# Performance work log

Measured on AMD Instinct MI355X. Metric: run time of the kernel, lower is better.

## Reference

```python
import jax, jax.numpy as jnp
import numpy as np

NEG_SLOPE = 0.2   # PyG GATConv default negative_slope
NUM_GRAPHS = 64   # graphs per batched timestep (max batch id + 1)


def setup_inputs() -> dict:
    key = jax.random.key(0)
    ks = jax.random.split(key, 16)
    T, N, E, F, H, C, B = 8, 20000, 320000, 128, 128, 16, NUM_GRAPHS
    x = jax.random.normal(ks[0], (T, N, F), dtype=jnp.float32)
    edge_index = jax.random.randint(ks[1], (T, 2, E), 0, N, dtype=jnp.int32)
    batch = jnp.sort(jax.random.randint(ks[2], (N,), 0, B, dtype=jnp.int32))
    z = jax.random.normal(ks[3], (B, H), dtype=jnp.float32)
    s_f = 1.0 / np.sqrt(F)
    s_h = 1.0 / np.sqrt(H)
    return {
        "x": x, "edge_index": edge_index, "batch": batch, "z": z,
        "gat_W": jax.random.normal(ks[4], (F, H), jnp.float32) * s_f,
        "att_src": jax.random.normal(ks[5], (H,), jnp.float32) * s_h,
        "att_dst": jax.random.normal(ks[6], (H,), jnp.float32) * s_h,
        "gat_bias": jnp.zeros((H,), jnp.float32),
        "W_ih": jax.random.normal(ks[7], (4 * H, H), jnp.float32) * s_h,
        "W_hh": jax.random.normal(ks[8], (4 * H, H), jnp.float32) * s_h,
        "b_ih": jnp.zeros((4 * H,), jnp.float32),
        "b_hh": jnp.zeros((4 * H,), jnp.float32),
        "fc_W": jax.random.normal(ks[9], (C, 2 * H), jnp.float32) * (1.0 / np.sqrt(2 * H)),
        "fc_b": jnp.zeros((C,), jnp.float32),
    }


def _gat_conv(x, edge_index, W, a_src, a_dst, bias):
    # PyG GATConv, heads=1, add_self_loops=True: gather -> softmax-per-target -> scatter
    N = x.shape[0]
    h = x @ W                                        # [N, H]
    loops = jnp.arange(N, dtype=edge_index.dtype)
    src = jnp.concatenate([edge_index[0], loops])    # message source j
    dst = jnp.concatenate([edge_index[1], loops])    # message target i
    e = jax.nn.leaky_relu((h @ a_src)[src] + (h @ a_dst)[dst], NEG_SLOPE)  # [E+N]
    m = jax.ops.segment_max(e, dst, num_segments=N)  # stable softmax over incoming edges
    w = jnp.exp(e - m[dst])
    denom = jax.ops.segment_sum(w, dst, num_segments=N)
    alpha = w / denom[dst]
    out = jax.ops.segment_sum(alpha[:, None] * h[src], dst, num_segments=N)
    return out + bias


def reference(x, edge_index, batch, z, gat_W, att_src, att_dst, gat_bias,
              W_ih, W_hh, b_ih, b_hh, fc_W, fc_b):
    B = NUM_GRAPHS
    # per-timestep GAT (vmapped over the window) + global mean pool
    node_feats = jax.vmap(lambda xt, ei: _gat_conv(xt, ei, gat_W, att_src, att_dst, gat_bias))(x, edge_index)  # [T,N,H]
    counts = jnp.maximum(jax.ops.segment_sum(jnp.ones_like(batch, jnp.float32), batch, num_segments=B), 1.0)
    pooled = jax.vmap(lambda f: jax.ops.segment_sum(f, batch, num_segments=B))(node_feats) / counts[None, :, None]  # [T,B,H]

    # LSTM over T (PyTorch gate order i, f, g, o)
    H = gat_W.shape[1]
    h0 = jnp.zeros((B, H), x.dtype)

    def step(carry, xt):
        h, c = carry
        gates = xt @ W_ih.T + b_ih + h @ W_hh.T + b_hh
        i, f, g, o = jnp.split(gates, 4, axis=-1)
        c = jax.nn.sigmoid(f) * c + jax.nn.sigmoid(i) * jnp.tanh(g)
        h = jax.nn.sigmoid(o) * jnp.tanh(c)
        return (h, c), None

    (h_n, _), _ = jax.lax.scan(step, (h0, h0), pooled)
    # dropout is identity at inference
    return jnp.concatenate([h_n, z], axis=1) @ fc_W.T + fc_b  # [B, num_classes]
```

## Files before the change

kernel.cpp:

```cpp
#include <hip/hip_runtime.h>
#include <math.h>

#define TT 8
#define NNODES 20000
#define NEDGES 320000
#define FDIM 128
#define HDIM 128
#define BGR 64
#define NCLS 16
#define NB 157
#define CB 80
#define EC 4000
#define CAP 2816

__device__ __forceinline__ float lrelu(float x) { return fmaxf(x, 0.2f * x); }
__device__ __forceinline__ float sigmoidf(float x) { return 1.0f / (1.0f + __expf(-x)); }
__device__ __forceinline__ float tanh_fast(float x) {
  return 1.0f - 2.0f / (__expf(2.0f * x) + 1.0f);
}
__device__ __forceinline__ unsigned short f2bf(float f) {
  unsigned int u = __float_as_uint(f);
  unsigned int r = (u + 0x7fff + ((u >> 16) & 1)) >> 16;
  return (unsigned short)r;
}
__device__ __forceinline__ float bf_lo(unsigned int u) { return __uint_as_float(u << 16); }
__device__ __forceinline__ float bf_hi(unsigned int u) { return __uint_as_float(u & 0xffff0000u); }

__global__ __launch_bounds__(256) void k_prep(
    const float* __restrict__ W, const float* __restrict__ att_s, const float* __restrict__ att_d,
    float* __restrict__ u, float* __restrict__ v) {
  const int tid = threadIdx.x;
  if (tid < 128) {
    float su = 0.f, sv = 0.f;
    const float4* wr = (const float4*)(W + (size_t)tid * 128);
    #pragma unroll 8
    for (int q = 0; q < 32; ++q) {
      float4 w4 = wr[q];
      float4 a4 = *(const float4*)(att_s + q * 4);
      float4 d4 = *(const float4*)(att_d + q * 4);
      su += w4.x * a4.x + w4.y * a4.y + w4.z * a4.z + w4.w * a4.w;
      sv += w4.x * d4.x + w4.y * d4.y + w4.z * d4.z + w4.w * d4.w;
    }
    u[tid] = su; v[tid] = sv;
  }
}

__global__ __launch_bounds__(256) void k_gemv(
    const float* __restrict__ x, const float* __restrict__ u, const float* __restrict__ v,
    float* __restrict__ as_, float* __restrict__ ad_, float* __restrict__ denom,
    unsigned int* __restrict__ xb) {
  const int tid = threadIdx.x;
  const int c4 = tid & 31;
  const int ty = tid >> 5;
  const int lane = tid & 63;
  float4 uu = *(const float4*)(u + c4 * 4);
  float4 vv = *(const float4*)(v + c4 * 4);
  const int base = blockIdx.x * 64;
  #pragma unroll
  for (int it = 0; it < 8; ++it) {
    int r = base + it * 8 + ty;
    float4 xv = *(const float4*)(x + (size_t)r * FDIM + c4 * 4);
    float ps = xv.x * uu.x + xv.y * uu.y + xv.z * uu.z + xv.w * uu.w;
    float pd = xv.x * vv.x + xv.y * vv.y + xv.z * vv.z + xv.w * vv.w;
    float4 px;
    px.x = __shfl_xor(xv.x, 16);
    px.y = __shfl_xor(xv.y, 16);
    px.z = __shfl_xor(xv.z, 16);
    px.w = __shfl_xor(xv.w, 16);
    if (c4 < 16) {
      uint4 pk;
      pk.x = (unsigned int)f2bf(xv.x) | ((unsigned int)f2bf(px.x) << 16);
      pk.y = (unsigned int)f2bf(xv.y) | ((unsigned int)f2bf(px.y) << 16);
      pk.z = (unsigned int)f2bf(xv.z) | ((unsigned int)f2bf(px.z) << 16);
      pk.w = (unsigned int)f2bf(xv.w) | ((unsigned int)f2bf(px.w) << 16);
      *(uint4*)(xb + (size_t)r * 64 + c4 * 4) = pk;
    }
    #pragma unroll
    for (int o = 16; o > 0; o >>= 1) { ps += __shfl_xor(ps, o); pd += __shfl_xor(pd, o); }
    if ((lane & 31) == 0) {
      as_[r] = ps;
      ad_[r] = pd;
      denom[r] = __expf(lrelu(ps + pd));
    }
  }
}

__global__ __launch_bounds__(256) void k_scat(
    const int* __restrict__ ei, int* __restrict__ cnt_d, int* __restrict__ cnt_s,
    unsigned int* __restrict__ part_d, unsigned int* __restrict__ part_s) {
  __shared__ unsigned int buf[EC];
  __shared__ int hd[NB], hs[NB];
  __shared__ int bd[NB], bs[NB];
  const int tid = threadIdx.x;
  const int chunk = blockIdx.x, t = blockIdx.y;
  if (tid < NB) { hd[tid] = 0; hs[tid] = 0; }
  __syncthreads();
  const int* eis = ei + (size_t)t * 2 * NEDGES;
  for (int i = tid; i < EC; i += 256) {
    int e = chunk * EC + i;
    int s = eis[e], d = eis[NEDGES + e];
    buf[i] = ((unsigned int)s << 15) | (unsigned int)d;
    atomicAdd(&hd[d >> 7], 1);
    atomicAdd(&hs[s >> 7], 1);
  }
  __syncthreads();
  if (tid < NB) {
    bd[tid] = atomicAdd(&cnt_d[t * NB + tid], hd[tid]);
    bs[tid] = atomicAdd(&cnt_s[t * NB + tid], hs[tid]);
    hd[tid] = 0; hs[tid] = 0;
  }
  __syncthreads();
  unsigned int* pdt = part_d + (size_t)t * NB * CAP;
  unsigned int* pst = part_s + (size_t)t * NB * CAP;
  for (int i = tid; i < EC; i += 256) {
    unsigned int rec = buf[i];
    int d = rec & 32767, s = rec >> 15;
    int Bd = d >> 7, Bs = s >> 7;
    int od = bd[Bd] + atomicAdd(&hd[Bd], 1);
    pdt[Bd * CAP + od] = rec;
    int os = bs[Bs] + atomicAdd(&hs[Bs], 1);
    pst[Bs * CAP + os] = rec;
  }
}

__global__ __launch_bounds__(256) void k_denomB(
    const unsigned int* __restrict__ part_d, const int* __restrict__ cnt_d,
    const float* __restrict__ as_, const float* __restrict__ ad_,
    const float* __restrict__ dseed, const int* __restrict__ batch,
    float4* __restrict__ aux4, int* __restrict__ starts) {
  __shared__ float hist[128];
  __shared__ float adl[128];
  const int tid = threadIdx.x;
  const int B = blockIdx.x, t = blockIdx.y;
  if (tid < 128) {
    hist[tid] = 0.f;
    int n = B * 128 + tid;
    adl[tid] = (n < NNODES) ? ad_[t * NNODES + n] : 0.f;
  }
  __syncthreads();
  const int cnt = cnt_d[t * NB + B];
  const unsigned int* pdt = part_d + ((size_t)t * NB + B) * CAP;
  const float* asb = as_ + (size_t)t * NNODES;
  int i = tid;
  for (; i + 768 < cnt; i += 1024) {
    unsigned int r0 = pdt[i], r1 = pdt[i + 256], r2 = pdt[i + 512], r3 = pdt[i + 768];
    float v0 = asb[r0 >> 15], v1 = asb[r1 >> 15], v2 = asb[r2 >> 15], v3 = asb[r3 >> 15];
    float w0 = __expf(lrelu(v0 + adl[r0 & 127]));
    float w1 = __expf(lrelu(v1 + adl[r1 & 127]));
    float w2 = __expf(lrelu(v2 + adl[r2 & 127]));
    float w3 = __expf(lrelu(v3 + adl[r3 & 127]));
    atomicAdd(&hist[r0 & 127], w0);
    atomicAdd(&hist[r1 & 127], w1);
    atomicAdd(&hist[r2 & 127], w2);
    atomicAdd(&hist[r3 & 127], w3);
  }
  for (; i < cnt; i += 256) {
    unsigned int rec = pdt[i];
    float w = __expf(lrelu(asb[rec >> 15] + adl[rec & 127]));
    atomicAdd(&hist[rec & 127], w);
  }
  __syncthreads();
  if (tid < 128) {
    int n = B * 128 + tid;
    if (n < NNODES) {
      float den = dseed[t * NNODES + n] + hist[tid];
      int bn = batch[n];
      aux4[t * NNODES + n] = make_float4(adl[tid], 1.0f / den, __int_as_float(bn), 0.f);
      if (t == 0) {
        if (n == 0) { for (int bb = 0; bb <= bn; ++bb) starts[bb] = 0; }
        else { int pb = batch[n - 1]; for (int bb = pb + 1; bb <= bn; ++bb) starts[bb] = n; }
        if (n == NNODES - 1) { for (int bb = bn + 1; bb <= BGR; ++bb) starts[bb] = NNODES; }
      }
    }
  }
}

__global__ __launch_bounds__(256) void k_cpgemm(
    const unsigned int* __restrict__ part_s, const int* __restrict__ cnt_s,
    const float* __restrict__ as_, const float4* __restrict__ aux4,
    const unsigned int* __restrict__ xb, unsigned int* __restrict__ ppart) {
  __shared__ float clT[128 * 64];
  const int tid = threadIdx.x;
  const int lane = tid & 63;
  const int B = blockIdx.x, t = blockIdx.y;
  #pragma unroll
  for (int i = tid; i < 128 * 64; i += 256) clT[i] = 0.f;
  const float* asb = as_ + (size_t)t * NNODES;
  float a0 = asb[min(B * 128 + lane, NNODES - 1)];
  float a1 = asb[min(B * 128 + 64 + lane, NNODES - 1)];
  __syncthreads();
  const float4* auxt = aux4 + (size_t)t * NNODES;
  if (tid < 128) {
    int n = B * 128 + tid;
    if (n < NNODES) {
      float4 aa = auxt[n];
      float wself = __expf(lrelu(asb[n] + aa.x)) * aa.y;
      atomicAdd(&clT[tid * 64 + __float_as_int(aa.z)], wself);
    }
  }
  {
    const int cnt = cnt_s[t * NB + B];
    const unsigned int* pst = part_s + ((size_t)t * NB + B) * CAP;
    int i = tid;
    for (; i + 768 < cnt; i += 1024) {
      unsigned int r0 = pst[i], r1 = pst[i + 256], r2 = pst[i + 512], r3 = pst[i + 768];
      float4 x0 = auxt[r0 & 32767], x1 = auxt[r1 & 32767];
      float4 x2 = auxt[r2 & 32767], x3 = auxt[r3 & 32767];
      int s0 = (int)(r0 >> 15) & 127, s1 = (int)(r1 >> 15) & 127;
      int s2 = (int)(r2 >> 15) & 127, s3 = (int)(r3 >> 15) & 127;
      float p0 = __shfl(a0, s0 & 63), q0 = __shfl(a1, s0 & 63);
      float p1 = __shfl(a0, s1 & 63), q1 = __shfl(a1, s1 & 63);
      float p2 = __shfl(a0, s2 & 63), q2 = __shfl(a1, s2 & 63);
      float p3 = __shfl(a0, s3 & 63), q3 = __shfl(a1, s3 & 63);
      float v0 = (s0 & 64) ? q0 : p0, v1 = (s1 & 64) ? q1 : p1;
      float v2 = (s2 & 64) ? q2 : p2, v3 = (s3 & 64) ? q3 : p3;
      float w0 = __expf(lrelu(v0 + x0.x)) * x0.y;
      float w1 = __expf(lrelu(v1 + x1.x)) * x1.y;
      float w2 = __expf(lrelu(v2 + x2.x)) * x2.y;
      float w3 = __expf(lrelu(v3 + x3.x)) * x3.y;
      atomicAdd(&clT[s0 * 64 + __float_as_int(x0.z)], w0);
      atomicAdd(&clT[s1 * 64 + __float_as_int(x1.z)], w1);
      atomicAdd(&clT[s2 * 64 + __float_as_int(x2.z)], w2);
      atomicAdd(&clT[s3 * 64 + __float_as_int(x3.z)], w3);
    }
    for (; i < cnt; i += 256) {
      unsigned int rec = pst[i];
      int s7 = (int)(rec >> 15) & 127;
      float4 aa = auxt[rec & 32767];
      float p = __shfl(a0, s7 & 63), q = __shfl(a1, s7 & 63);
      float v = (s7 & 64) ? q : p;
      float w = __expf(lrelu(v + aa.x)) * aa.y;
      atomicAdd(&clT[s7 * 64 + __float_as_int(aa.z)], w);
    }
  }
  __syncthreads();
  const int bq = tid >> 4;
  const int dq = tid & 15;
  const unsigned int* xrow = xb + (size_t)t * NNODES * 64;
  float acc[4][8] = {};
  #pragma unroll 4
  for (int kk = 0; kk < 128; ++kk) {
    int row = B * 128 + kk;
    row = (row < NNODES) ? row : (NNODES - 1);
    uint4 u4 = *(const uint4*)(xrow + (size_t)row * 64 + dq * 4);
    float xd[8];
    xd[0] = bf_lo(u4.x); xd[4] = bf_hi(u4.x);
    xd[1] = bf_lo(u4.y); xd[5] = bf_hi(u4.y);
    xd[2] = bf_lo(u4.z); xd[6] = bf_hi(u4.z);
    xd[3] = bf_lo(u4.w); xd[7] = bf_hi(u4.w);
    float cv[4];
    *(float4*)cv = *(const float4*)&clT[kk * 64 + bq * 4];
    #pragma unroll
    for (int i = 0; i < 4; ++i)
      #pragma unroll
      for (int d = 0; d < 8; ++d)
        acc[i][d] += cv[i] * xd[d];
  }
  unsigned int* pp = ppart + ((size_t)t * NB + B) * BGR * 64;
  #pragma unroll
  for (int i = 0; i < 4; ++i) {
    uint4 pk;
    pk.x = (unsigned int)f2bf(acc[i][0]) | ((unsigned int)f2bf(acc[i][4]) << 16);
    pk.y = (unsigned int)f2bf(acc[i][1]) | ((unsigned int)f2bf(acc[i][5]) << 16);
    pk.z = (unsigned int)f2bf(acc[i][2]) | ((unsigned int)f2bf(acc[i][6]) << 16);
    pk.w = (unsigned int)f2bf(acc[i][3]) | ((unsigned int)f2bf(acc[i][7]) << 16);
    *(uint4*)(pp + (bq * 4 + i) * 64 + dq * 4) = pk;
  }
}

__global__ __launch_bounds__(128) void k_pw(
    const unsigned int* __restrict__ ppart, const int* __restrict__ starts,
    const float* __restrict__ W, const float* __restrict__ gat_bias,
    float* __restrict__ pooled) {
  __shared__ float srow[128];
  const int tb = blockIdx.x;
  const int t = tb >> 6, b = tb & 63;
  const int d = threadIdx.x;
  if (d < 64) {
    float slo = 0.f, shi = 0.f;
    const unsigned int* pp = ppart + ((size_t)t * NB * BGR + b) * 64 + d;
    #pragma unroll 4
    for (int B = 0; B < NB; ++B) {
      unsigned int u = pp[(size_t)B * BGR * 64];
      slo += bf_lo(u); shi += bf_hi(u);
    }
    srow[d] = slo; srow[64 + d] = shi;
  }
  __syncthreads();
  const float invc = 1.0f / (float)max(starts[b + 1] - starts[b], 1);
  float o = 0.f;
  #pragma unroll 8
  for (int k = 0; k < 128; ++k) o += srow[k] * W[k * 128 + d];
  pooled[(size_t)(t * BGR + b) * HDIM + d] = o * invc + gat_bias[d];
}

__global__ __launch_bounds__(512) void k_lstm_fc(
    const float* __restrict__ pooled,
    const float* __restrict__ W_ih, const float* __restrict__ W_hh,
    const float* __restrict__ b_ih, const float* __restrict__ b_hh,
    const float* __restrict__ z, const float* __restrict__ fc_W,
    const float* __restrict__ fc_b, float* __restrict__ out) {
  const int b = blockIdx.x;
  const int g = threadIdx.x;
  __shared__ unsigned int wpk[512 * 65];
  __shared__ float hv[128], cv[128], part[512];
  __shared__ float pool8[TT][128];
  __shared__ float fcp[16][17];

  #pragma unroll 2
  for (int it = 0; it < 64; ++it) {
    int i = g + it * 512;
    int gr = i >> 6, j = i & 63;
    float2 wv = *(const float2*)(W_hh + (size_t)gr * HDIM + j * 2);
    wpk[gr * 65 + j] = (unsigned int)f2bf(wv.x) | ((unsigned int)f2bf(wv.y) << 16);
  }
  #pragma unroll
  for (int i = 0; i < 2; ++i) {
    int idx = g + i * 512;
    int t = idx >> 7, k = idx & 127;
    pool8[t][k] = pooled[((size_t)t * BGR + b) * HDIM + k];
  }
  if (g < 128) { hv[g] = 0.f; cv[g] = 0.f; }
  __syncthreads();

  float gx[8] = {};
  {
    const float4* wi = (const float4*)(W_ih + (size_t)g * HDIM);
    #pragma unroll 2
    for (int k4 = 0; k4 < 32; ++k4) {
      float4 wv = wi[k4];
      #pragma unroll
      for (int t = 0; t < TT; ++t) {
        float4 p = *(const float4*)(&pool8[t][k4 * 4]);
        gx[t] += wv.x * p.x + wv.y * p.y + wv.z * p.z + wv.w * p.w;
      }
    }
  }
  const float bsum = b_ih[g] + b_hh[g];
  const unsigned int* wr = &wpk[g * 65];
  const float4* hv4 = (const float4*)hv;
  #pragma unroll
  for (int t = 0; t < TT; ++t) {
    float s = gx[t] + bsum;
    #pragma unroll 8
    for (int j2 = 0; j2 < 32; ++j2) {
      unsigned int w0 = wr[2 * j2], w1 = wr[2 * j2 + 1];
      float4 hh = hv4[j2];
      s += bf_lo(w0) * hh.x + bf_hi(w0) * hh.y + bf_lo(w1) * hh.z + bf_hi(w1) * hh.w;
    }
    part[g] = s;
    __syncthreads();
    if (g < 128) {
      float ig = sigmoidf(part[g]);
      float fg = sigmoidf(part[128 + g]);
      float gc = tanh_fast(part[256 + g]);
      float og = sigmoidf(part[384 + g]);
      float c = fg * cv[g] + ig * gc;
      cv[g] = c;
      hv[g] = og * tanh_fast(c);
    }
    __syncthreads();
  }
  if (g < 256) {
    const int c = g >> 4, kp = g & 15;
    float s = 0.f;
    for (int k = kp * 16; k < kp * 16 + 16; ++k) {
      float v = (k < 128) ? hv[k] : z[(size_t)b * HDIM + (k - 128)];
      s += v * fc_W[(size_t)c * 256 + k];
    }
    fcp[c][kp] = s;
  }
  __syncthreads();
  if (g < 16) {
    float r = fc_b[g];
    #pragma unroll
    for (int k = 0; k < 16; ++k) r += fcp[g][k];
    out[(size_t)b * NCLS + g] = r;
  }
}

extern "C" void kernel_launch(void* const* d_in, const int* in_sizes, int n_in,
                              void* d_out, int out_size, void* d_ws, size_t ws_size,
                              hipStream_t stream) {
  const float* x       = (const float*)d_in[0];
  const int*   ei      = (const int*)d_in[1];
  const int*   batch   = (const int*)d_in[2];
  const float* z       = (const float*)d_in[3];
  const float* gat_W   = (const float*)d_in[4];
  const float* att_src = (const float*)d_in[5];
  const float* att_dst = (const float*)d_in[6];
  const float* gat_bias= (const float*)d_in[7];
  const float* W_ih    = (const float*)d_in[8];
  const float* W_hh    = (const float*)d_in[9];
  const float* b_ih    = (const float*)d_in[10];
  const float* b_hh    = (const float*)d_in[11];
  const float* fc_W    = (const float*)d_in[12];
  const float* fc_b    = (const float*)d_in[13];
  float* out = (float*)d_out;

  char* ws = (char*)d_ws;
  size_t off = 0;
  auto alloc = [&](size_t bytes) {
    void* p = (void*)(ws + off);
    off += (bytes + 255) & ~(size_t)255;
    return p;
  };
  float*  as_    = (float*)alloc((size_t)TT * NNODES * 4);
  float*  ad_    = (float*)alloc((size_t)TT * NNODES * 4);
  float*  denom  = (float*)alloc((size_t)TT * NNODES * 4);
  float4* aux4   = (float4*)alloc((size_t)TT * NNODES * 16);
  int*    cnt2   = (int*)alloc((size_t)2 * TT * NB * 4);
  int*    cnt_d  = cnt2;
  int*    cnt_s  = cnt2 + TT * NB;
  unsigned int* part_d = (unsigned int*)alloc(((size_t)TT * NB + 1) * CAP * 4);
  unsigned int* part_s = (unsigned int*)alloc(((size_t)TT * NB + 1) * CAP * 4);
  unsigned int* ppart  = (unsigned int*)alloc((size_t)TT * NB * BGR * 64 * 4);
  unsigned int* xb     = (unsigned int*)alloc((size_t)TT * NNODES * 64 * 4);
  float* uvec  = (float*)alloc(128 * 4);
  float* vvec  = (float*)alloc(128 * 4);
  float* pooled = (float*)alloc((size_t)TT * BGR * HDIM * 4);
  int* starts = (int*)alloc((BGR + 1) * 4);
  (void)ws_size; (void)in_sizes; (void)n_in; (void)out_size;

  hipMemsetAsync(cnt2, 0, (size_t)2 * TT * NB * 4, stream);

  k_prep<<<1, 256, 0, stream>>>(gat_W, att_src, att_dst, uvec, vvec);
  k_gemv<<<(TT * NNODES) / 64, 256, 0, stream>>>(x, uvec, vvec, as_, ad_, denom, xb);
  k_scat<<<dim3(CB, TT), 256, 0, stream>>>(ei, cnt_d, cnt_s, part_d, part_s);
  k_denomB<<<dim3(NB, TT), 256, 0, stream>>>(part_d, cnt_d, as_, ad_, denom, batch, aux4, starts);
  k_cpgemm<<<dim3(NB, TT), 256, 0, stream>>>(part_s, cnt_s, as_, aux4, xb, ppart);
  k_pw<<<TT * BGR, 128, 0, stream>>>(ppart, starts, gat_W, gat_bias, pooled);
  k_lstm_fc<<<BGR, 512, 0, stream>>>(pooled, W_ih, W_hh, b_ih, b_hh, z, fc_W, fc_b, out);
}
```

Baseline: 202.7 us.

## Merge gemv and edge scatter into one launch and halve node bucket size

```diff
diff --git a/kernel.cpp b/kernel.cpp
--- a/kernel.cpp
+++ b/kernel.cpp
@@ -8,10 +8,11 @@
 #define HDIM 128
 #define BGR 64
 #define NCLS 16
-#define NB 157
+#define NB 313
 #define CB 80
 #define EC 4000
-#define CAP 2816
+#define CAP 1536
+#define GGEMV 2500
 
 __device__ __forceinline__ float lrelu(float x) { return fmaxf(x, 0.2f * x); }
 __device__ __forceinline__ float sigmoidf(float x) { return 1.0f / (1.0f + __expf(-x)); }
@@ -45,81 +46,81 @@
   }
 }
 
-__global__ __launch_bounds__(256) void k_gemv(
+__global__ __launch_bounds__(256) void k_front(
     const float* __restrict__ x, const float* __restrict__ u, const float* __restrict__ v,
     float* __restrict__ as_, float* __restrict__ ad_, float* __restrict__ denom,
-    unsigned int* __restrict__ xb) {
-  const int tid = threadIdx.x;
-  const int c4 = tid & 31;
-  const int ty = tid >> 5;
-  const int lane = tid & 63;
-  float4 uu = *(const float4*)(u + c4 * 4);
-  float4 vv = *(const float4*)(v + c4 * 4);
-  const int base = blockIdx.x * 64;
-  #pragma unroll
-  for (int it = 0; it < 8; ++it) {
-    int r = base + it * 8 + ty;
-    float4 xv = *(const float4*)(x + (size_t)r * FDIM + c4 * 4);
-    float ps = xv.x * uu.x + xv.y * uu.y + xv.z * uu.z + xv.w * uu.w;
-    float pd = xv.x * vv.x + xv.y * vv.y + xv.z * vv.z + xv.w * vv.w;
-    float4 px;
-    px.x = __shfl_xor(xv.x, 16);
-    px.y = __shfl_xor(xv.y, 16);
-    px.z = __shfl_xor(xv.z, 16);
-    px.w = __shfl_xor(xv.w, 16);
-    if (c4 < 16) {
-      uint4 pk;
-      pk.x = (unsigned int)f2bf(xv.x) | ((unsigned int)f2bf(px.x) << 16);
-      pk.y = (unsigned int)f2bf(xv.y) | ((unsigned int)f2bf(px.y) << 16);
-      pk.z = (unsigned int)f2bf(xv.z) | ((unsigned int)f2bf(px.z) << 16);
-      pk.w = (unsigned int)f2bf(xv.w) | ((unsigned int)f2bf(px.w) << 16);
-      *(uint4*)(xb + (size_t)r * 64 + c4 * 4) = pk;
-    }
-    #pragma unroll
-    for (int o = 16; o > 0; o >>= 1) { ps += __shfl_xor(ps, o); pd += __shfl_xor(pd, o); }
-    if ((lane & 31) == 0) {
-      as_[r] = ps;
-      ad_[r] = pd;
-      denom[r] = __expf(lrelu(ps + pd));
-    }
-  }
-}
-
-__global__ __launch_bounds__(256) void k_scat(
+    unsigned int* __restrict__ xb,
     const int* __restrict__ ei, int* __restrict__ cnt_d, int* __restrict__ cnt_s,
     unsigned int* __restrict__ part_d, unsigned int* __restrict__ part_s) {
   __shared__ unsigned int buf[EC];
   __shared__ int hd[NB], hs[NB];
   __shared__ int bd[NB], bs[NB];
   const int tid = threadIdx.x;
-  const int chunk = blockIdx.x, t = blockIdx.y;
-  if (tid < NB) { hd[tid] = 0; hs[tid] = 0; }
-  __syncthreads();
-  const int* eis = ei + (size_t)t * 2 * NEDGES;
-  for (int i = tid; i < EC; i += 256) {
-    int e = chunk * EC + i;
-    int s = eis[e], d = eis[NEDGES + e];
-    buf[i] = ((unsigned int)s << 15) | (unsigned int)d;
-    atomicAdd(&hd[d >> 7], 1);
-    atomicAdd(&hs[s >> 7], 1);
-  }
-  __syncthreads();
-  if (tid < NB) {
-    bd[tid] = atomicAdd(&cnt_d[t * NB + tid], hd[tid]);
-    bs[tid] = atomicAdd(&cnt_s[t * NB + tid], hs[tid]);
-    hd[tid] = 0; hs[tid] = 0;
-  }
-  __syncthreads();
-  unsigned int* pdt = part_d + (size_t)t * NB * CAP;
-  unsigned int* pst = part_s + (size_t)t * NB * CAP;
-  for (int i = tid; i < EC; i += 256) {
-    unsigned int rec = buf[i];
-    int d = rec & 32767, s = rec >> 15;
-    int Bd = d >> 7, Bs = s >> 7;
-    int od = bd[Bd] + atomicAdd(&hd[Bd], 1);
-    pdt[Bd * CAP + od] = rec;
-    int os = bs[Bs] + atomicAdd(&hs[Bs], 1);
-    pst[Bs * CAP + os] = rec;
+  if (blockIdx.x < GGEMV) {
+    const int c4 = tid & 31;
+    const int ty = tid >> 5;
+    const int lane = tid & 63;
+    float4 uu = *(const float4*)(u + c4 * 4);
+    float4 vv = *(const float4*)(v + c4 * 4);
+    const int base = blockIdx.x * 64;
+    #pragma unroll
+    for (int it = 0; it < 8; ++it) {
+      int r = base + it * 8 + ty;
+      float4 xv = *(const float4*)(x + (size_t)r * FDIM + c4 * 4);
+      float ps = xv.x * uu.x + xv.y * uu.y + xv.z * uu.z + xv.w * uu.w;
+      float pd = xv.x * vv.x + xv.y * vv.y + xv.z * vv.z + xv.w * vv.w;
+      float4 px;
+      px.x = __shfl_xor(xv.x, 16);
+      px.y = __shfl_xor(xv.y, 16);
+      px.z = __shfl_xor(xv.z, 16);
+      px.w = __shfl_xor(xv.w, 16);
+      if (c4 < 16) {
+        uint4 pk;
+        pk.x = (unsigned int)f2bf(xv.x) | ((unsigned int)f2bf(px.x) << 16);
+        pk.y = (unsigned int)f2bf(xv.y) | ((unsigned int)f2bf(px.y) << 16);
+        pk.z = (unsigned int)f2bf(xv.z) | ((unsigned int)f2bf(px.z) << 16);
+        pk.w = (unsigned int)f2bf(xv.w) | ((unsigned int)f2bf(px.w) << 16);
+        *(uint4*)(xb + (size_t)r * 64 + c4 * 4) = pk;
+      }
+      #pragma unroll
+      for (int o = 16; o > 0; o >>= 1) { ps += __shfl_xor(ps, o); pd += __shfl_xor(pd, o); }
+      if ((lane & 31) == 0) {
+        as_[r] = ps;
+        ad_[r] = pd;
+        denom[r] = __expf(lrelu(ps + pd));
+      }
+    }
+  } else {
+    const int idx = blockIdx.x - GGEMV;
+    const int chunk = idx % CB, t = idx / CB;
+    for (int i = tid; i < NB; i += 256) { hd[i] = 0; hs[i] = 0; }
+    __syncthreads();
+    const int* eis = ei + (size_t)t * 2 * NEDGES;
+    for (int i = tid; i < EC; i += 256) {
+      int e = chunk * EC + i;
+      int s = eis[e], d = eis[NEDGES + e];
+      buf[i] = ((unsigned int)s << 15) | (unsigned int)d;
+      atomicAdd(&hd[d >> 6], 1);
+      atomicAdd(&hs[s >> 6], 1);
+    }
+    __syncthreads();
+    for (int i = tid; i < NB; i += 256) {
+      bd[i] = atomicAdd(&cnt_d[t * NB + i], hd[i]);
+      bs[i] = atomicAdd(&cnt_s[t * NB + i], hs[i]);
+      hd[i] = 0; hs[i] = 0;
+    }
+    __syncthreads();
+    unsigned int* pdt = part_d + (size_t)t * NB * CAP;
+    unsigned int* pst = part_s + (size_t)t * NB * CAP;
+    for (int i = tid; i < EC; i += 256) {
+      unsigned int rec = buf[i];
+      int d = rec & 32767, s = rec >> 15;
+      int Bd = d >> 6, Bs = s >> 6;
+      int od = bd[Bd] + atomicAdd(&hd[Bd], 1);
+      pdt[Bd * CAP + od] = rec;
+      int os = bs[Bs] + atomicAdd(&hs[Bs], 1);
+      pst[Bs * CAP + os] = rec;
+    }
   }
 }
 
@@ -128,13 +129,13 @@
     const float* __restrict__ as_, const float* __restrict__ ad_,
     const float* __restrict__ dseed, const int* __restrict__ batch,
     float4* __restrict__ aux4, int* __restrict__ starts) {
-  __shared__ float hist[128];
-  __shared__ float adl[128];
+  __shared__ float hist[64];
+  __shared__ float adl[64];
   const int tid = threadIdx.x;
   const int B = blockIdx.x, t = blockIdx.y;
-  if (tid < 128) {
+  if (tid < 64) {
     hist[tid] = 0.f;
-    int n = B * 128 + tid;
+    int n = B * 64 + tid;
     adl[tid] = (n < NNODES) ? ad_[t * NNODES + n] : 0.f;
   }
   __syncthreads();
@@ -145,23 +146,23 @@
   for (; i + 768 < cnt; i += 1024) {
     unsigned int r0 = pdt[i], r1 = pdt[i + 256], r2 = pdt[i + 512], r3 = pdt[i + 768];
     float v0 = asb[r0 >> 15], v1 = asb[r1 >> 15], v2 = asb[r2 >> 15], v3 = asb[r3 >> 15];
-    float w0 = __expf(lrelu(v0 + adl[r0 & 127]));
-    float w1 = __expf(lrelu(v1 + adl[r1 & 127]));
-    float w2 = __expf(lrelu(v2 + adl[r2 & 127]));
-    float w3 = __expf(lrelu(v3 + adl[r3 & 127]));
-    atomicAdd(&hist[r0 & 127], w0);
-    atomicAdd(&hist[r1 & 127], w1);
-    atomicAdd(&hist[r2 & 127], w2);
-    atomicAdd(&hist[r3 & 127], w3);
+    float w0 = __expf(lrelu(v0 + adl[r0 & 63]));
+    float w1 = __expf(lrelu(v1 + adl[r1 & 63]));
+    float w2 = __expf(lrelu(v2 + adl[r2 & 63]));
+    float w3 = __expf(lrelu(v3 + adl[r3 & 63]));
+    atomicAdd(&hist[r0 & 63], w0);
+    atomicAdd(&hist[r1 & 63], w1);
+    atomicAdd(&hist[r2 & 63], w2);
+    atomicAdd(&hist[r3 & 63], w3);
   }
   for (; i < cnt; i += 256) {
     unsigned int rec = pdt[i];
-    float w = __expf(lrelu(asb[rec >> 15] + adl[rec & 127]));
-    atomicAdd(&hist[rec & 127], w);
-  }
-  __syncthreads();
-  if (tid < 128) {
-    int n = B * 128 + tid;
+    float w = __expf(lrelu(asb[rec >> 15] + adl[rec & 63]));
+    atomicAdd(&hist[rec & 63], w);
+  }
+  __syncthreads();
+  if (tid < 64) {
+    int n = B * 64 + tid;
     if (n < NNODES) {
       float den = dseed[t * NNODES + n] + hist[tid];
       int bn = batch[n];
@@ -179,19 +180,18 @@
     const unsigned int* __restrict__ part_s, const int* __restrict__ cnt_s,
     const float* __restrict__ as_, const float4* __restrict__ aux4,
     const unsigned int* __restrict__ xb, unsigned int* __restrict__ ppart) {
-  __shared__ float clT[128 * 64];
+  __shared__ float clT[64 * 64];
   const int tid = threadIdx.x;
   const int lane = tid & 63;
   const int B = blockIdx.x, t = blockIdx.y;
   #pragma unroll
-  for (int i = tid; i < 128 * 64; i += 256) clT[i] = 0.f;
+  for (int i = tid; i < 64 * 64; i += 256) clT[i] = 0.f;
   const float* asb = as_ + (size_t)t * NNODES;
-  float a0 = asb[min(B * 128 + lane, NNODES - 1)];
-  float a1 = asb[min(B * 128 + 64 + lane, NNODES - 1)];
+  float a0 = asb[min(B * 64 + lane, NNODES - 1)];
   __syncthreads();
   const float4* auxt = aux4 + (size_t)t * NNODES;
-  if (tid < 128) {
-    int n = B * 128 + tid;
+  if (tid < 64) {
+    int n = B * 64 + tid;
     if (n < NNODES) {
       float4 aa = auxt[n];
       float wself = __expf(lrelu(asb[n] + aa.x)) * aa.y;
@@ -206,14 +206,10 @@
       unsigned int r0 = pst[i], r1 = pst[i + 256], r2 = pst[i + 512], r3 = pst[i + 768];
       float4 x0 = auxt[r0 & 32767], x1 = auxt[r1 & 32767];
       float4 x2 = auxt[r2 & 32767], x3 = auxt[r3 & 32767];
-      int s0 = (int)(r0 >> 15) & 127, s1 = (int)(r1 >> 15) & 127;
-      int s2 = (int)(r2 >> 15) & 127, s3 = (int)(r3 >> 15) & 127;
-      float p0 = __shfl(a0, s0 & 63), q0 = __shfl(a1, s0 & 63);
-      float p1 = __shfl(a0, s1 & 63), q1 = __shfl(a1, s1 & 63);
-      float p2 = __shfl(a0, s2 & 63), q2 = __shfl(a1, s2 & 63);
-      float p3 = __shfl(a0, s3 & 63), q3 = __shfl(a1, s3 & 63);
-      float v0 = (s0 & 64) ? q0 : p0, v1 = (s1 & 64) ? q1 : p1;
-      float v2 = (s2 & 64) ? q2 : p2, v3 = (s3 & 64) ? q3 : p3;
+      int s0 = (int)(r0 >> 15) & 63, s1 = (int)(r1 >> 15) & 63;
+      int s2 = (int)(r2 >> 15) & 63, s3 = (int)(r3 >> 15) & 63;
+      float v0 = __shfl(a0, s0), v1 = __shfl(a0, s1);
+      float v2 = __shfl(a0, s2), v3 = __shfl(a0, s3);
       float w0 = __expf(lrelu(v0 + x0.x)) * x0.y;
       float w1 = __expf(lrelu(v1 + x1.x)) * x1.y;
       float w2 = __expf(lrelu(v2 + x2.x)) * x2.y;
@@ -225,12 +221,11 @@
     }
     for (; i < cnt; i += 256) {
       unsigned int rec = pst[i];
-      int s7 = (int)(rec >> 15) & 127;
+      int s6 = (int)(rec >> 15) & 63;
       float4 aa = auxt[rec & 32767];
-      float p = __shfl(a0, s7 & 63), q = __shfl(a1, s7 & 63);
-      float v = (s7 & 64) ? q : p;
+      float v = __shfl(a0, s6);
       float w = __expf(lrelu(v + aa.x)) * aa.y;
-      atomicAdd(&clT[s7 * 64 + __float_as_int(aa.z)], w);
+      atomicAdd(&clT[s6 * 64 + __float_as_int(aa.z)], w);
     }
   }
   __syncthreads();
@@ -239,8 +234,8 @@
   const unsigned int* xrow = xb + (size_t)t * NNODES * 64;
   float acc[4][8] = {};
   #pragma unroll 4
-  for (int kk = 0; kk < 128; ++kk) {
-    int row = B * 128 + kk;
+  for (int kk = 0; kk < 64; ++kk) {
+    int row = B * 64 + kk;
     row = (row < NNODES) ? row : (NNODES - 1);
     uint4 u4 = *(const uint4*)(xrow + (size_t)row * 64 + dq * 4);
     float xd[8];
@@ -425,8 +420,8 @@
   hipMemsetAsync(cnt2, 0, (size_t)2 * TT * NB * 4, stream);
 
   k_prep<<<1, 256, 0, stream>>>(gat_W, att_src, att_dst, uvec, vvec);
-  k_gemv<<<(TT * NNODES) / 64, 256, 0, stream>>>(x, uvec, vvec, as_, ad_, denom, xb);
-  k_scat<<<dim3(CB, TT), 256, 0, stream>>>(ei, cnt_d, cnt_s, part_d, part_s);
+  k_front<<<GGEMV + CB * TT, 256, 0, stream>>>(x, uvec, vvec, as_, ad_, denom, xb,
+                                               ei, cnt_d, cnt_s, part_d, part_s);
   k_denomB<<<dim3(NB, TT), 256, 0, stream>>>(part_d, cnt_d, as_, ad_, denom, batch, aux4, starts);
   k_cpgemm<<<dim3(NB, TT), 256, 0, stream>>>(part_s, cnt_s, as_, aux4, xb, ppart);
   k_pw<<<TT * BGR, 128, 0, stream>>>(ppart, starts, gat_W, gat_bias, pooled);
```

New measurement: 218.0 us. 7.6% more time.
